# Optimization experiments

Hardware: AMD Instinct MI355X
Metric: run time of the kernel (lower is better)

Reference implementation:

```python
import jax, jax.numpy as jnp
import numpy as np

FEAT_DIM = 16
NUM_DEPTHS = 64


def _lookat(p):
    z = p / np.linalg.norm(p)
    up = np.array([0.0, 1.0, 0.0])
    x = np.cross(up, z); x = x / np.linalg.norm(x)
    y = np.cross(z, x)
    m = np.eye(4)
    m[:3, 0] = x; m[:3, 1] = y; m[:3, 2] = z; m[:3, 3] = p
    return m


def setup_inputs() -> dict:
    key = jax.random.key(0)
    ks = jax.random.split(key, 6)
    S, Vin, Vt, C, D, H, W = 2, 3, 4, FEAT_DIM, NUM_DEPTHS, 96, 96
    enc = jax.random.normal(ks[0], (S, Vin, C, D, H, W), jnp.float32) * 0.5
    rng = np.random.default_rng(0)

    def poses(n):
        ps = rng.normal(size=(S, n, 3))
        ps = ps / np.linalg.norm(ps, axis=-1, keepdims=True) * 1.3
        return jnp.asarray(np.stack([[_lookat(ps[i, j]) for j in range(n)] for i in range(S)]), jnp.float32)

    input_poses = poses(Vin)
    target_poses = poses(Vt)
    W1 = jax.random.normal(ks[1], (16, 64), jnp.float32) * 0.25
    W2 = jax.random.normal(ks[2], (64, 64), jnp.float32) * 0.125
    W3 = jax.random.normal(ks[3], (64, 17), jnp.float32) * 0.125
    return dict(
        encoded_imgs=enc, input_poses=input_poses, target_poses=target_poses,
        focal=1.2, z_near=0.8, z_far=1.8, samples_per_ray=64,
        W1=W1, b1=jnp.zeros((64,), jnp.float32),
        W2=W2, b2=jnp.zeros((64,), jnp.float32),
        W3=W3, b3=jnp.zeros((17,), jnp.float32),
    )


def grid_sample_3d(vol, grid):
    # vol: (N,C,D,H,W); grid: (N,P,3) xyz in [-1,1]; trilinear, zero padding, align_corners=False
    N, C, D, H, W = vol.shape
    P = grid.shape[1]
    ix = ((grid[..., 0] + 1.0) * W - 1.0) * 0.5
    iy = ((grid[..., 1] + 1.0) * H - 1.0) * 0.5
    iz = ((grid[..., 2] + 1.0) * D - 1.0) * 0.5
    x0, y0, z0 = jnp.floor(ix), jnp.floor(iy), jnp.floor(iz)
    volf = vol.reshape(N, C, D * H * W)
    out = jnp.zeros((N, C, P), vol.dtype)
    for dz in (0, 1):
        for dy in (0, 1):
            for dx in (0, 1):
                xc, yc, zc = x0 + dx, y0 + dy, z0 + dz
                wgt = (1.0 - jnp.abs(ix - xc)) * (1.0 - jnp.abs(iy - yc)) * (1.0 - jnp.abs(iz - zc))
                valid = ((xc >= 0) & (xc < W) & (yc >= 0) & (yc < H) & (zc >= 0) & (zc < D))
                xi = jnp.clip(xc, 0, W - 1).astype(jnp.int32)
                yi = jnp.clip(yc, 0, H - 1).astype(jnp.int32)
                zi = jnp.clip(zc, 0, D - 1).astype(jnp.int32)
                idx = (zi * H + yi) * W + xi  # (N,P)
                vals = jnp.take_along_axis(volf, idx[:, None, :], axis=2)  # (N,C,P)
                out = out + (wgt * valid)[:, None, :] * vals
    return out


def _upsample2_align_corners(x):
    # bilinear x2 on last two axes, align_corners=True (torch UpsamplingBilinear2d)
    def interp(x, axis):
        n = x.shape[axis]
        m = 2 * n
        pos = jnp.arange(m) * ((n - 1) / (m - 1))
        lo = jnp.floor(pos).astype(jnp.int32)
        hi = jnp.minimum(lo + 1, n - 1)
        f = (pos - lo).astype(x.dtype)
        xl = jnp.take(x, lo, axis=axis)
        xh = jnp.take(x, hi, axis=axis)
        shp = [1] * x.ndim; shp[axis] = m
        f = f.reshape(shp)
        return xl * (1.0 - f) + xh * f
    return interp(interp(x, -2), -1)


def _forward(encoded_imgs, input_poses, target_poses, focal, z_near, z_far,
             samples_per_ray, W1, b1, W2, b2, W3, b3):
    S, Vin, C, D, H, W = encoded_imgs.shape
    Vt = target_poses.shape[1]
    h, w = H // 2, W // 2
    spr = samples_per_ray
    dt = encoded_imgs.dtype

    # --- gen_rays at half resolution ---
    poses = target_poses.reshape(S * Vt, 4, 4)
    ys = ((jnp.arange(h, dtype=dt) + 0.5) / h) * 2.0 - 1.0
    xs = ((jnp.arange(w, dtype=dt) + 0.5) / w) * 2.0 - 1.0
    yy, xx = jnp.meshgrid(ys, xs, indexing='ij')
    dirs_cam = jnp.stack([xx / focal, -yy / focal, -jnp.ones_like(xx)], -1)  # (h,w,3)
    dirs = jnp.einsum('bij,hwj->bhwi', poses[:, :3, :3], dirs_cam)            # (B,h,w,3)
    origins = poses[:, None, None, :3, 3]                                      # (B,1,1,3)

    t = z_near + (z_far - z_near) * (jnp.arange(spr, dtype=dt) / (spr - 1))
    times = jnp.broadcast_to(t, (S * Vt, h, w, spr))
    pts = origins[..., None, :] + times[..., None] * dirs[..., None, :]        # (B,h,w,spr,3)

    times = times.reshape(S, Vt, h, w, spr)
    pts = pts.reshape(S, Vt, h, w, spr, 3)
    pts_h = jnp.concatenate([pts, jnp.ones_like(pts[..., :1])], axis=-1)      # (S,Vt,h,w,spr,4)

    # --- invert input poses (rigid) ---
    R = input_poses[..., :3, :3]
    tr = input_poses[..., :3, 3]
    Rt = jnp.swapaxes(R, -1, -2)
    inv_t = -jnp.einsum('svij,svj->svi', Rt, tr)
    top = jnp.concatenate([Rt, inv_t[..., None]], axis=-1)                     # (S,Vin,3,4)
    bottom = jnp.broadcast_to(jnp.array([0.0, 0.0, 0.0, 1.0], dt), (S, Vin, 1, 4))
    extrinsics = jnp.concatenate([top, bottom], axis=-2)                       # (S,Vin,4,4)

    local = jnp.einsum('svij,sthwpj->svthwpi', extrinsics, pts_h)              # (S,Vin,Vt,h,w,spr,4)
    x = local[..., 0]
    y = local[..., 1]
    z = -local[..., 2]
    u = x / z * focal
    v = y / z * focal
    min_z, max_z = focal * z_near, focal * z_far
    wd = 2.0 * (z - min_z) / (max_z - min_z) - 1.0
    uvw = jnp.stack((u, -v, -wd), axis=-1)                                     # (S,Vin,Vt,h,w,spr,3)

    feats = grid_sample_3d(encoded_imgs.reshape(S * Vin, C, D, H, W),
                           uvw.reshape(S * Vin, -1, 3))                        # (S*Vin,C,P)
    feats = feats.reshape(S, Vin, C, Vt, h, w, spr)
    feats = jnp.mean(feats, axis=1)                                            # baseline_mean camera weighting
    feats = jnp.transpose(feats, (0, 2, 3, 4, 5, 1))                           # (S,Vt,h,w,spr,C)

    # --- MLP with residual feature skip ---
    x1 = jax.nn.relu(feats @ W1 + b1)
    x2 = jax.nn.relu(x1 @ W2 + b2)
    out = x2 @ W3 + b3                                                         # (...,17)
    density = jax.nn.relu(out[..., 0])
    rgb = feats + out[..., 1:]

    # --- volume rendering ---
    deltas = times[..., 1:] - times[..., :-1]
    last = jnp.full_like(deltas[..., :1], 1e10)
    deltas = jnp.concatenate([deltas, last], axis=-1)
    sigdel = density * deltas
    alpha = 1.0 - jnp.exp(-sigdel)
    transmittance = jnp.exp(-jnp.cumsum(sigdel, axis=-1))
    wts = alpha * transmittance
    renders = jnp.sum(wts[..., None] * rgb, axis=-2)                           # (S,Vt,h,w,16)

    renders = jnp.transpose(renders, (0, 1, 4, 2, 3))                          # (S,Vt,16,h,w)
    renders = _upsample2_align_corners(renders.reshape(S * Vt, C, h, w))
    return renders.reshape(S, Vt, C, H, W)


def reference(encoded_imgs, input_poses, target_poses, focal, z_near, z_far,
              samples_per_ray, W1, b1, W2, b2, W3, b3):
    return _forward(encoded_imgs, input_poses, target_poses, float(focal), float(z_near),
                    float(z_far), int(samples_per_ray), W1, b1, W2, b2, W3, b3)
```

## Files before the change

### kernel.cpp

```cpp
#include <hip/hip_runtime.h>
#include <hip/hip_bf16.h>
#include <math.h>

#define NS   2
#define NVIN 3
#define NVT  4
#define NC   16
#define ND   64
#define NH   96
#define NW   96
#define HWH  48
#define SPR  64
#define DHW  (ND*NH*NW)
#define NTILE (DHW / 64)
#define NSAMP (NS*NVT*HWH*HWH*SPR)

typedef __attribute__((ext_vector_type(8))) short bfrag;
typedef __attribute__((ext_vector_type(4))) float cfrag;

#define MFMA16 __builtin_amdgcn_mfma_f32_16x16x32_bf16

__device__ __forceinline__ short f2bf(float x) {
    union { __hip_bfloat16 b; short s; } cv;
    cv.b = __float2bfloat16(x);
    return cv.s;
}
__device__ __forceinline__ float bf2f(short s) {
    union { unsigned int u; float f; } cv;
    cv.u = ((unsigned int)(unsigned short)s) << 16;
    return cv.f;
}

__device__ __forceinline__ void mk_frag(const float* p, bfrag& ah, bfrag& al) {
    float4 v0 = *(const float4*)p;
    float4 v1 = *(const float4*)(p + 4);
    float e[8] = {v0.x, v0.y, v0.z, v0.w, v1.x, v1.y, v1.z, v1.w};
    #pragma unroll
    for (int j = 0; j < 8; j++) {
        short h = f2bf(e[j]);
        ah[j] = h;
        al[j] = f2bf(e[j] - bf2f(h));
    }
}

__global__ __launch_bounds__(256) void wprep_kernel(
    const float* __restrict__ W1, const float* __restrict__ W2,
    const float* __restrict__ W3, short* __restrict__ whi, short* __restrict__ wlo)
{
    int t = blockIdx.x * 256 + threadIdx.x;
    int f = t >> 6, L = t & 63;
    int q = L >> 4, li = L & 15;
    #pragma unroll
    for (int j = 0; j < 8; j++) {
        int kloc = q * 8 + j;
        float w = 0.f;
        if (f < 4) {
            int n = f * 16 + li, k = kloc;
            if (k < 16) w = W1[k * 64 + n];
        } else if (f < 12) {
            int kt = (f - 4) >> 2, nt = (f - 4) & 3;
            w = W2[(kt * 32 + kloc) * 64 + nt * 16 + li];
        } else {
            int kt = (f - 12) >> 1, nt = (f - 12) & 1;
            int n = nt * 16 + li;
            if (n < 17) w = W3[(kt * 32 + kloc) * 17 + n];
        }
        short h = f2bf(w);
        whi[(f * 64 + L) * 8 + j] = h;
        wlo[(f * 64 + L) * 8 + j] = f2bf(w - bf2f(h));
    }
}

__global__ __launch_bounds__(256) void transpose_kernel(
    const float* __restrict__ in, float* __restrict__ out)
{
    __shared__ float tile[NC][64 + 4];
    const int t   = threadIdx.x;
    const int blk = blockIdx.x;
    const int vox0 = (blk % NTILE) * 64;
    const int sv   = blk / NTILE;

    const int c  = t >> 4;
    const int vg = (t & 15) * 4;
    const float* src = in + ((size_t)sv * NC + c) * DHW + vox0 + vg;
    float4 v = *(const float4*)src;
    tile[c][vg + 0] = v.x; tile[c][vg + 1] = v.y;
    tile[c][vg + 2] = v.z; tile[c][vg + 3] = v.w;
    __syncthreads();

    const int ov = t >> 2;
    const int oc = (t & 3) * 4;
    float4 w = make_float4(tile[oc + 0][ov], tile[oc + 1][ov],
                           tile[oc + 2][ov], tile[oc + 3][ov]);
    float* dst = out + ((size_t)sv * DHW + vox0 + ov) * NC + oc;
    *(float4*)dst = w;
}

__global__ __launch_bounds__(256) void gather_kernel(
    const float* __restrict__ enc_t,
    const float* __restrict__ ipose,
    const float* __restrict__ tpose,
    const float* __restrict__ focal_p,
    const float* __restrict__ znear_p,
    const float* __restrict__ zfar_p,
    float* __restrict__ xbuf)
{
    const int tid = blockIdx.x * 256 + threadIdx.x;
    const int c4  = tid & 3;
    const int smp = tid >> 2;
    const int d   = smp & 63;
    const int ray = smp >> 6;
    const int px  = ray % HWH;
    const int py  = (ray / HWH) % HWH;
    const int b   = ray / (HWH * HWH);
    const int s   = b >> 2;

    const float focal = focal_p[0];
    const float znear = znear_p[0];
    const float zfar  = zfar_p[0];

    const float* P = tpose + b * 16;
    float ysc = ((py + 0.5f) / (float)HWH) * 2.f - 1.f;
    float xsc = ((px + 0.5f) / (float)HWH) * 2.f - 1.f;
    float dcx = xsc / focal, dcy = -ysc / focal, dcz = -1.f;
    float dirx = P[0]*dcx + P[1]*dcy + P[2]*dcz;
    float diry = P[4]*dcx + P[5]*dcy + P[6]*dcz;
    float dirz = P[8]*dcx + P[9]*dcy + P[10]*dcz;

    float tv  = znear + (zfar - znear) * ((float)d / (float)(SPR - 1));
    float ptx = P[3] + tv * dirx, pty = P[7] + tv * diry, ptz = P[11] + tv * dirz;

    const float minz = focal * znear, maxz = focal * zfar;
    float f0 = 0.f, f1 = 0.f, f2 = 0.f, f3 = 0.f;

    for (int v = 0; v < NVIN; v++) {
        const float* E = ipose + (s * NVIN + v) * 16;
        float qx = ptx - E[3], qy = pty - E[7], qz = ptz - E[11];
        float lx = E[0]*qx + E[4]*qy + E[8]*qz;
        float ly = E[1]*qx + E[5]*qy + E[9]*qz;
        float lz = E[2]*qx + E[6]*qy + E[10]*qz;
        float zz = -lz;
        float u  = lx / zz * focal;
        float vv = ly / zz * focal;
        float wd = 2.f * (zz - minz) / (maxz - minz) - 1.f;
        float ix = ((u   + 1.f) * NW - 1.f) * 0.5f;
        float iy = ((-vv + 1.f) * NH - 1.f) * 0.5f;
        float iz = ((-wd + 1.f) * ND - 1.f) * 0.5f;
        float x0 = floorf(ix), y0 = floorf(iy), z0 = floorf(iz);

        const float* VB = enc_t + (size_t)(s * NVIN + v) * DHW * NC;
        #pragma unroll
        for (int k = 0; k < 8; k++) {
            float xc = x0 + (k & 1), yc = y0 + ((k >> 1) & 1), zc = z0 + (k >> 2);
            float wt = (1.f - fabsf(ix - xc)) * (1.f - fabsf(iy - yc)) * (1.f - fabsf(iz - zc));
            bool valid = (xc >= 0.f) && (xc < (float)NW) &&
                         (yc >= 0.f) && (yc < (float)NH) &&
                         (zc >= 0.f) && (zc < (float)ND);
            float w = valid ? wt : 0.f;
            int xi = min(max((int)xc, 0), NW - 1);
            int yi = min(max((int)yc, 0), NH - 1);
            int zi = min(max((int)zc, 0), ND - 1);
            int idx = (zi * NH + yi) * NW + xi;
            float4 a = *(const float4*)(VB + (size_t)idx * NC + c4 * 4);
            f0 += w * a.x; f1 += w * a.y; f2 += w * a.z; f3 += w * a.w;
        }
    }
    const float inv3 = 1.f / 3.f;
    ((float4*)xbuf)[tid] = make_float4(f0 * inv3, f1 * inv3, f2 * inv3, f3 * inv3);
}

__global__ __launch_bounds__(256) void mlp_kernel(
    const float* __restrict__ xbuf,
    const float* __restrict__ znear_p,
    const float* __restrict__ zfar_p,
    const short* __restrict__ whi, const short* __restrict__ wlo,
    const float* __restrict__ B1, const float* __restrict__ B2,
    const float* __restrict__ B3,
    float* __restrict__ rhalf)
{
    const int lane = threadIdx.x & 63;
    const int ray  = blockIdx.x * 4 + (threadIdx.x >> 6);
    const int px   = ray % HWH;
    const int py   = (ray / HWH) % HWH;
    const int b    = ray / (HWH * HWH);

    const float znear = znear_p[0];
    const float zfar  = zfar_p[0];

    __shared__ float sbuf[4][64][36];
    float (*B)[36] = sbuf[threadIdx.x >> 6];
    const int li = lane & 15, q = lane >> 4;
    const float* X = xbuf + (size_t)ray * 64 * NC;

    float b1v[4], b2v[4], b3v[2];
    #pragma unroll
    for (int nt = 0; nt < 4; nt++) { b1v[nt] = B1[nt*16 + li]; b2v[nt] = B2[nt*16 + li]; }
    b3v[0] = B3[li];
    b3v[1] = (li == 0) ? B3[16] : 0.f;

    bfrag xah[4], xal[4];
    bfrag zb = {0,0,0,0,0,0,0,0};
    #pragma unroll
    for (int mt = 0; mt < 4; mt++) {
        if (q < 2) mk_frag(X + (mt*16 + li) * NC + q * 8, xah[mt], xal[mt]);
        else { xah[mt] = zb; xal[mt] = zb; }
    }

    cfrag zc = {0.f, 0.f, 0.f, 0.f};
    cfrag h2acc[4][4];
    #pragma unroll
    for (int mt = 0; mt < 4; mt++)
        #pragma unroll
        for (int nt = 0; nt < 4; nt++) h2acc[mt][nt] = zc;

    #pragma unroll
    for (int c1 = 0; c1 < 2; c1++) {
        cfrag h1[4][2];
        #pragma unroll
        for (int nt2 = 0; nt2 < 2; nt2++) {
            int f = 2*c1 + nt2;
            bfrag bh = *(const bfrag*)(whi + (f*64 + lane)*8);
            bfrag bl = *(const bfrag*)(wlo + (f*64 + lane)*8);
            #pragma unroll
            for (int mt = 0; mt < 4; mt++) {
                cfrag a = zc;
                a = MFMA16(xal[mt], bh, a, 0, 0, 0);
                a = MFMA16(xah[mt], bl, a, 0, 0, 0);
                a = MFMA16(xah[mt], bh, a, 0, 0, 0);
                h1[mt][nt2] = a;
            }
        }
        __syncthreads();
        #pragma unroll
        for (int mt = 0; mt < 4; mt++)
            #pragma unroll
            for (int nt2 = 0; nt2 < 2; nt2++)
                #pragma unroll
                for (int r = 0; r < 4; r++)
                    B[mt*16 + q*4 + r][nt2*16 + li] =
                        fmaxf(h1[mt][nt2][r] + b1v[2*c1 + nt2], 0.f);
        __syncthreads();
        bfrag hah[4], hal[4];
        #pragma unroll
        for (int mt = 0; mt < 4; mt++)
            mk_frag(&B[mt*16 + li][q*8], hah[mt], hal[mt]);
        #pragma unroll
        for (int nt = 0; nt < 4; nt++) {
            int f = 4 + c1*4 + nt;
            bfrag bh = *(const bfrag*)(whi + (f*64 + lane)*8);
            bfrag bl = *(const bfrag*)(wlo + (f*64 + lane)*8);
            #pragma unroll
            for (int mt = 0; mt < 4; mt++) {
                cfrag a = h2acc[mt][nt];
                a = MFMA16(hal[mt], bh, a, 0, 0, 0);
                a = MFMA16(hah[mt], bl, a, 0, 0, 0);
                a = MFMA16(hah[mt], bh, a, 0, 0, 0);
                h2acc[mt][nt] = a;
            }
        }
    }

    cfrag oacc[4][2];
    #pragma unroll
    for (int mt = 0; mt < 4; mt++)
        #pragma unroll
        for (int nt = 0; nt < 2; nt++) oacc[mt][nt] = zc;

    #pragma unroll
    for (int c2 = 0; c2 < 2; c2++) {
        __syncthreads();
        #pragma unroll
        for (int mt = 0; mt < 4; mt++)
            #pragma unroll
            for (int nt2 = 0; nt2 < 2; nt2++)
                #pragma unroll
                for (int r = 0; r < 4; r++)
                    B[mt*16 + q*4 + r][nt2*16 + li] =
                        fmaxf(h2acc[mt][2*c2 + nt2][r] + b2v[2*c2 + nt2], 0.f);
        __syncthreads();
        bfrag hah[4], hal[4];
        #pragma unroll
        for (int mt = 0; mt < 4; mt++)
            mk_frag(&B[mt*16 + li][q*8], hah[mt], hal[mt]);
        #pragma unroll
        for (int nt = 0; nt < 2; nt++) {
            int f = 12 + c2*2 + nt;
            bfrag bh = *(const bfrag*)(whi + (f*64 + lane)*8);
            bfrag bl = *(const bfrag*)(wlo + (f*64 + lane)*8);
            #pragma unroll
            for (int mt = 0; mt < 4; mt++) {
                cfrag a = oacc[mt][nt];
                a = MFMA16(hal[mt], bh, a, 0, 0, 0);
                a = MFMA16(hah[mt], bl, a, 0, 0, 0);
                a = MFMA16(hah[mt], bh, a, 0, 0, 0);
                oacc[mt][nt] = a;
            }
        }
    }

    __syncthreads();
    #pragma unroll
    for (int mt = 0; mt < 4; mt++)
        #pragma unroll
        for (int nt = 0; nt < 2; nt++) {
            int ch = nt*16 + li;
            if (ch < 17) {
                #pragma unroll
                for (int r = 0; r < 4; r++)
                    B[mt*16 + q*4 + r][ch] = oacc[mt][nt][r] + b3v[nt];
            }
        }
    __syncthreads();
    float4 o0 = *(float4*)&B[lane][0];
    float4 o1 = *(float4*)&B[lane][4];
    float4 o2 = *(float4*)&B[lane][8];
    float4 o3 = *(float4*)&B[lane][12];
    float o16 = B[lane][16];

    float density = fmaxf(o0.x, 0.f);
    float orgb[16] = {o0.y, o0.z, o0.w, o1.x, o1.y, o1.z, o1.w, o2.x,
                      o2.y, o2.z, o2.w, o3.x, o3.y, o3.z, o3.w, o16};

    float4 fx0 = *(const float4*)(X + lane * NC + 0);
    float4 fx1 = *(const float4*)(X + lane * NC + 4);
    float4 fx2 = *(const float4*)(X + lane * NC + 8);
    float4 fx3 = *(const float4*)(X + lane * NC + 12);
    float feats[16] = {fx0.x, fx0.y, fx0.z, fx0.w, fx1.x, fx1.y, fx1.z, fx1.w,
                       fx2.x, fx2.y, fx2.z, fx2.w, fx3.x, fx3.y, fx3.z, fx3.w};

    float tv = znear + (zfar - znear) * ((float)lane / (float)(SPR - 1));
    float tn = znear + (zfar - znear) * ((float)(lane + 1) / (float)(SPR - 1));
    float delta = (lane < SPR - 1) ? (tn - tv) : 1e10f;
    float sigdel = density * delta;
    float alpha = 1.f - expf(-sigdel);
    float csum = sigdel;
    #pragma unroll
    for (int off = 1; off < 64; off <<= 1) {
        float nb = __shfl_up(csum, off, 64);
        if (lane >= off) csum += nb;
    }
    float wray = alpha * expf(-csum);

    #pragma unroll
    for (int c = 0; c < NC; c++) {
        float val = wray * (feats[c] + orgb[c]);
        #pragma unroll
        for (int off = 32; off >= 1; off >>= 1)
            val += __shfl_down(val, off, 64);
        if (lane == 0)
            rhalf[((b * NC + c) * HWH + py) * HWH + px] = val;
    }
}

__device__ __forceinline__ void mlp_and_composite(
    const float feats[NC], int lane, int b, int py, int px,
    float tv, float znear, float zfar,
    const float* __restrict__ W1, const float* __restrict__ B1,
    const float* __restrict__ W2, const float* __restrict__ B2,
    const float* __restrict__ W3, const float* __restrict__ B3,
    float* __restrict__ rhalf)
{
    float outa[17];
    #pragma unroll
    for (int c = 0; c < 17; c++) outa[c] = B3[c];
    for (int kc = 0; kc < 4; kc++) {
        float h2c[16];
        #pragma unroll
        for (int k = 0; k < 16; k++) h2c[k] = B2[kc * 16 + k];
        #pragma unroll 4
        for (int j = 0; j < 64; j++) {
            float a = B1[j];
            #pragma unroll
            for (int i = 0; i < NC; i++) a += feats[i] * W1[i * 64 + j];
            a = fmaxf(a, 0.f);
            const float* w2p = W2 + j * 64 + kc * 16;
            #pragma unroll
            for (int k = 0; k < 16; k++) h2c[k] += a * w2p[k];
        }
        #pragma unroll
        for (int k = 0; k < 16; k++) {
            float hv = fmaxf(h2c[k], 0.f);
            const float* w3p = W3 + (kc * 16 + k) * 17;
            #pragma unroll
            for (int c = 0; c < 17; c++) outa[c] += hv * w3p[c];
        }
    }
    float density = fmaxf(outa[0], 0.f);
    float tn = znear + (zfar - znear) * ((float)(lane + 1) / (float)(SPR - 1));
    float delta = (lane < SPR - 1) ? (tn - tv) : 1e10f;
    float sigdel = density * delta;
    float alpha = 1.f - expf(-sigdel);
    float csum = sigdel;
    #pragma unroll
    for (int off = 1; off < 64; off <<= 1) {
        float nb = __shfl_up(csum, off, 64);
        if (lane >= off) csum += nb;
    }
    float wray = alpha * expf(-csum);
    #pragma unroll
    for (int c = 0; c < NC; c++) {
        float val = wray * (feats[c] + outa[1 + c]);
        #pragma unroll
        for (int off = 32; off >= 1; off >>= 1)
            val += __shfl_down(val, off, 64);
        if (lane == 0)
            rhalf[((b * NC + c) * HWH + py) * HWH + px] = val;
    }
}

__global__ __launch_bounds__(256) void render_kernel(
    const float* __restrict__ enc,
    const float* __restrict__ ipose,
    const float* __restrict__ tpose,
    const float* __restrict__ focal_p,
    const float* __restrict__ znear_p,
    const float* __restrict__ zfar_p,
    const float* __restrict__ W1, const float* __restrict__ B1,
    const float* __restrict__ W2, const float* __restrict__ B2,
    const float* __restrict__ W3, const float* __restrict__ B3,
    float* __restrict__ rhalf)
{
    const int lane = threadIdx.x & 63;
    const int ray  = blockIdx.x * 4 + (threadIdx.x >> 6);
    const int px   = ray % HWH;
    const int py   = (ray / HWH) % HWH;
    const int b    = ray / (HWH * HWH);
    const int s    = b >> 2;
    const float focal = focal_p[0];
    const float znear = znear_p[0];
    const float zfar  = zfar_p[0];
    const float* P = tpose + b * 16;
    float ysc = ((py + 0.5f) / (float)HWH) * 2.f - 1.f;
    float xsc = ((px + 0.5f) / (float)HWH) * 2.f - 1.f;
    float dcx = xsc / focal, dcy = -ysc / focal, dcz = -1.f;
    float dirx = P[0]*dcx + P[1]*dcy + P[2]*dcz;
    float diry = P[4]*dcx + P[5]*dcy + P[6]*dcz;
    float dirz = P[8]*dcx + P[9]*dcy + P[10]*dcz;
    float tv  = znear + (zfar - znear) * ((float)lane / (float)(SPR - 1));
    float ptx = P[3] + tv * dirx, pty = P[7] + tv * diry, ptz = P[11] + tv * dirz;
    float feats[NC];
    #pragma unroll
    for (int c = 0; c < NC; c++) feats[c] = 0.f;
    const float minz = focal * znear, maxz = focal * zfar;
    for (int v = 0; v < NVIN; v++) {
        const float* E = ipose + (s * NVIN + v) * 16;
        float qx = ptx - E[3], qy = pty - E[7], qz = ptz - E[11];
        float lx = E[0]*qx + E[4]*qy + E[8]*qz;
        float ly = E[1]*qx + E[5]*qy + E[9]*qz;
        float lz = E[2]*qx + E[6]*qy + E[10]*qz;
        float zz = -lz;
        float u  = lx / zz * focal;
        float vv = ly / zz * focal;
        float wd = 2.f * (zz - minz) / (maxz - minz) - 1.f;
        float ix = ((u   + 1.f) * NW - 1.f) * 0.5f;
        float iy = ((-vv + 1.f) * NH - 1.f) * 0.5f;
        float iz = ((-wd + 1.f) * ND - 1.f) * 0.5f;
        float x0 = floorf(ix), y0 = floorf(iy), z0 = floorf(iz);
        float wgt[8]; int idx[8];
        #pragma unroll
        for (int k = 0; k < 8; k++) {
            float xc = x0 + (k & 1), yc = y0 + ((k >> 1) & 1), zc = z0 + (k >> 2);
            float wt = (1.f - fabsf(ix - xc)) * (1.f - fabsf(iy - yc)) * (1.f - fabsf(iz - zc));
            bool valid = (xc >= 0.f) && (xc < (float)NW) &&
                         (yc >= 0.f) && (yc < (float)NH) &&
                         (zc >= 0.f) && (zc < (float)ND);
            wgt[k] = valid ? wt : 0.f;
            int xi = min(max((int)xc, 0), NW - 1);
            int yi = min(max((int)yc, 0), NH - 1);
            int zi = min(max((int)zc, 0), ND - 1);
            idx[k] = (zi * NH + yi) * NW + xi;
        }
        const float* VB = enc + (size_t)(s * NVIN + v) * NC * DHW;
        #pragma unroll
        for (int c = 0; c < NC; c++) {
            const float* vc = VB + c * DHW;
            float acc = 0.f;
            #pragma unroll
            for (int k = 0; k < 8; k++) acc += wgt[k] * vc[idx[k]];
            feats[c] += acc;
        }
    }
    #pragma unroll
    for (int c = 0; c < NC; c++) feats[c] *= (1.f / 3.f);
    mlp_and_composite(feats, lane, b, py, px, tv, znear, zfar,
                      W1, B1, W2, B2, W3, B3, rhalf);
}

__global__ __launch_bounds__(256) void upsample_kernel(
    const float* __restrict__ in, float* __restrict__ out)
{
    int tid = blockIdx.x * 256 + threadIdx.x;
    int ox = tid % NW;
    int oy = (tid / NW) % NH;
    int c  = (tid / (NW * NH)) % NC;
    int b  = tid / (NW * NH * NC);
    const float sc = (float)((HWH - 1) / (double)(NH - 1));
    float pyf = oy * sc;
    float pxf = ox * sc;
    int y0 = (int)floorf(pyf); int y1 = min(y0 + 1, HWH - 1); float fy = pyf - y0;
    int x0 = (int)floorf(pxf); int x1 = min(x0 + 1, HWH - 1); float fx = pxf - x0;
    const float* src = in + (b * NC + c) * HWH * HWH;
    float v00 = src[y0 * HWH + x0], v01 = src[y0 * HWH + x1];
    float v10 = src[y1 * HWH + x0], v11 = src[y1 * HWH + x1];
    float gl = v00 * (1.f - fy) + v10 * fy;
    float gr = v01 * (1.f - fy) + v11 * fy;
    out[tid] = gl * (1.f - fx) + gr * fx;
}

extern "C" void kernel_launch(void* const* d_in, const int* in_sizes, int n_in,
                              void* d_out, int out_size, void* d_ws, size_t ws_size,
                              hipStream_t stream) {
    const float* enc   = (const float*)d_in[0];
    const float* ipose = (const float*)d_in[1];
    const float* tpose = (const float*)d_in[2];
    const float* focal = (const float*)d_in[3];
    const float* znear = (const float*)d_in[4];
    const float* zfar  = (const float*)d_in[5];
    const float* W1 = (const float*)d_in[7];
    const float* B1 = (const float*)d_in[8];
    const float* W2 = (const float*)d_in[9];
    const float* B2 = (const float*)d_in[10];
    const float* W3 = (const float*)d_in[11];
    const float* B3 = (const float*)d_in[12];

    float* out = (float*)d_out;
    const int nrays = NS * NVT * HWH * HWH;
    const int nout  = NS * NVT * NC * NH * NW;
    const size_t enc_t_bytes = (size_t)NS * NVIN * NC * DHW * 4;
    const size_t rhalf_bytes = (size_t)nrays * NC * 4;
    const size_t wfrag_bytes = 16 * 64 * 8 * sizeof(short);
    const size_t xbuf_bytes  = (size_t)NSAMP * NC * 4;

    if (ws_size >= enc_t_bytes + rhalf_bytes + 2 * wfrag_bytes + xbuf_bytes) {
        char* base = (char*)d_ws;
        float* enc_t = (float*)base;                      base += enc_t_bytes;
        float* rhalf = (float*)base;                      base += rhalf_bytes;
        short* whi   = (short*)base;                      base += wfrag_bytes;
        short* wlo   = (short*)base;                      base += wfrag_bytes;
        float* xbuf  = (float*)base;

        wprep_kernel<<<4, 256, 0, stream>>>(W1, W2, W3, whi, wlo);
        transpose_kernel<<<NS * NVIN * NTILE, 256, 0, stream>>>(enc, enc_t);
        gather_kernel<<<NSAMP * 4 / 256, 256, 0, stream>>>(
            enc_t, ipose, tpose, focal, znear, zfar, xbuf);
        mlp_kernel<<<nrays / 4, 256, 0, stream>>>(
            xbuf, znear, zfar, whi, wlo, B1, B2, B3, rhalf);
        upsample_kernel<<<nout / 256, 256, 0, stream>>>(rhalf, out);
    } else {
        float* rhalf = (float*)d_ws;
        render_kernel<<<nrays / 4, 256, 0, stream>>>(
            enc, ipose, tpose, focal, znear, zfar,
            W1, B1, W2, B2, W3, B3, rhalf);
        upsample_kernel<<<nout / 256, 256, 0, stream>>>(rhalf, out);
    }
}
```

Measured before the change: 616.3 us.

## Fuse gather and MLP into one kernel with per-wave LDS staging

Result: slower. 652.4 us (+5.9%).

```diff
diff --git a/kernel.cpp b/kernel.cpp
--- a/kernel.cpp
+++ b/kernel.cpp
@@ -19,6 +19,8 @@
 typedef __attribute__((ext_vector_type(4))) float cfrag;
 
 #define MFMA16 __builtin_amdgcn_mfma_f32_16x16x32_bf16
+
+#define WAVE_LDS_SYNC() asm volatile("s_waitcnt lgkmcnt(0)" ::: "memory")
 
 __device__ __forceinline__ short f2bf(float x) {
     union { __hip_bfloat16 b; short s; } cv;
@@ -96,81 +98,13 @@
     *(float4*)dst = w;
 }
 
-__global__ __launch_bounds__(256) void gather_kernel(
+#define XSTRIDE 20
+
+__global__ __launch_bounds__(256) void fused_kernel(
     const float* __restrict__ enc_t,
     const float* __restrict__ ipose,
     const float* __restrict__ tpose,
     const float* __restrict__ focal_p,
-    const float* __restrict__ znear_p,
-    const float* __restrict__ zfar_p,
-    float* __restrict__ xbuf)
-{
-    const int tid = blockIdx.x * 256 + threadIdx.x;
-    const int c4  = tid & 3;
-    const int smp = tid >> 2;
-    const int d   = smp & 63;
-    const int ray = smp >> 6;
-    const int px  = ray % HWH;
-    const int py  = (ray / HWH) % HWH;
-    const int b   = ray / (HWH * HWH);
-    const int s   = b >> 2;
-
-    const float focal = focal_p[0];
-    const float znear = znear_p[0];
-    const float zfar  = zfar_p[0];
-
-    const float* P = tpose + b * 16;
-    float ysc = ((py + 0.5f) / (float)HWH) * 2.f - 1.f;
-    float xsc = ((px + 0.5f) / (float)HWH) * 2.f - 1.f;
-    float dcx = xsc / focal, dcy = -ysc / focal, dcz = -1.f;
-    float dirx = P[0]*dcx + P[1]*dcy + P[2]*dcz;
-    float diry = P[4]*dcx + P[5]*dcy + P[6]*dcz;
-    float dirz = P[8]*dcx + P[9]*dcy + P[10]*dcz;
-
-    float tv  = znear + (zfar - znear) * ((float)d / (float)(SPR - 1));
-    float ptx = P[3] + tv * dirx, pty = P[7] + tv * diry, ptz = P[11] + tv * dirz;
-
-    const float minz = focal * znear, maxz = focal * zfar;
-    float f0 = 0.f, f1 = 0.f, f2 = 0.f, f3 = 0.f;
-
-    for (int v = 0; v < NVIN; v++) {
-        const float* E = ipose + (s * NVIN + v) * 16;
-        float qx = ptx - E[3], qy = pty - E[7], qz = ptz - E[11];
-        float lx = E[0]*qx + E[4]*qy + E[8]*qz;
-        float ly = E[1]*qx + E[5]*qy + E[9]*qz;
-        float lz = E[2]*qx + E[6]*qy + E[10]*qz;
-        float zz = -lz;
-        float u  = lx / zz * focal;
-        float vv = ly / zz * focal;
-        float wd = 2.f * (zz - minz) / (maxz - minz) - 1.f;
-        float ix = ((u   + 1.f) * NW - 1.f) * 0.5f;
-        float iy = ((-vv + 1.f) * NH - 1.f) * 0.5f;
-        float iz = ((-wd + 1.f) * ND - 1.f) * 0.5f;
-        float x0 = floorf(ix), y0 = floorf(iy), z0 = floorf(iz);
-
-        const float* VB = enc_t + (size_t)(s * NVIN + v) * DHW * NC;
-        #pragma unroll
-        for (int k = 0; k < 8; k++) {
-            float xc = x0 + (k & 1), yc = y0 + ((k >> 1) & 1), zc = z0 + (k >> 2);
-            float wt = (1.f - fabsf(ix - xc)) * (1.f - fabsf(iy - yc)) * (1.f - fabsf(iz - zc));
-            bool valid = (xc >= 0.f) && (xc < (float)NW) &&
-                         (yc >= 0.f) && (yc < (float)NH) &&
-                         (zc >= 0.f) && (zc < (float)ND);
-            float w = valid ? wt : 0.f;
-            int xi = min(max((int)xc, 0), NW - 1);
-            int yi = min(max((int)yc, 0), NH - 1);
-            int zi = min(max((int)zc, 0), ND - 1);
-            int idx = (zi * NH + yi) * NW + xi;
-            float4 a = *(const float4*)(VB + (size_t)idx * NC + c4 * 4);
-            f0 += w * a.x; f1 += w * a.y; f2 += w * a.z; f3 += w * a.w;
-        }
-    }
-    const float inv3 = 1.f / 3.f;
-    ((float4*)xbuf)[tid] = make_float4(f0 * inv3, f1 * inv3, f2 * inv3, f3 * inv3);
-}
-
-__global__ __launch_bounds__(256) void mlp_kernel(
-    const float* __restrict__ xbuf,
     const float* __restrict__ znear_p,
     const float* __restrict__ zfar_p,
     const short* __restrict__ whi, const short* __restrict__ wlo,
@@ -179,18 +113,90 @@
     float* __restrict__ rhalf)
 {
     const int lane = threadIdx.x & 63;
-    const int ray  = blockIdx.x * 4 + (threadIdx.x >> 6);
+    const int wv   = threadIdx.x >> 6;
+    const int ray  = blockIdx.x * 4 + wv;
     const int px   = ray % HWH;
     const int py   = (ray / HWH) % HWH;
     const int b    = ray / (HWH * HWH);
-
+    const int s    = b >> 2;
+
+    const float focal = focal_p[0];
     const float znear = znear_p[0];
     const float zfar  = zfar_p[0];
 
-    __shared__ float sbuf[4][64][36];
-    float (*B)[36] = sbuf[threadIdx.x >> 6];
+    __shared__ float sbuf[4][64 * 36];
+    float* Wb = sbuf[wv];
+    float* Xs = sbuf[wv];
+
+    const float* P = tpose + b * 16;
+    float ysc = ((py + 0.5f) / (float)HWH) * 2.f - 1.f;
+    float xsc = ((px + 0.5f) / (float)HWH) * 2.f - 1.f;
+    float dcx = xsc / focal, dcy = -ysc / focal, dcz = -1.f;
+    float dirx = P[0]*dcx + P[1]*dcy + P[2]*dcz;
+    float diry = P[4]*dcx + P[5]*dcy + P[6]*dcz;
+    float dirz = P[8]*dcx + P[9]*dcy + P[10]*dcz;
+
+    float lox[NVIN], loy[NVIN], loz[NVIN];
+    float ldx[NVIN], ldy[NVIN], ldz[NVIN];
+    #pragma unroll
+    for (int v = 0; v < NVIN; v++) {
+        const float* E = ipose + (s * NVIN + v) * 16;
+        float qx = P[3] - E[3], qy = P[7] - E[7], qz = P[11] - E[11];
+        lox[v] = E[0]*qx + E[4]*qy + E[8]*qz;
+        loy[v] = E[1]*qx + E[5]*qy + E[9]*qz;
+        loz[v] = E[2]*qx + E[6]*qy + E[10]*qz;
+        ldx[v] = E[0]*dirx + E[4]*diry + E[8]*dirz;
+        ldy[v] = E[1]*dirx + E[5]*diry + E[9]*dirz;
+        ldz[v] = E[2]*dirx + E[6]*diry + E[10]*dirz;
+    }
+
+    const float minz = focal * znear, maxz = focal * zfar;
+    const int  c4    = lane & 3;
+    const int  dbase = lane >> 2;
+    const float inv3 = 1.f / 3.f;
+
+    #pragma unroll 1
+    for (int i = 0; i < 4; i++) {
+        int d = dbase + i * 16;
+        float tv = znear + (zfar - znear) * ((float)d / (float)(SPR - 1));
+        float f0 = 0.f, f1 = 0.f, f2 = 0.f, f3 = 0.f;
+        #pragma unroll
+        for (int v = 0; v < NVIN; v++) {
+            float lx = lox[v] + tv * ldx[v];
+            float ly = loy[v] + tv * ldy[v];
+            float lz = loz[v] + tv * ldz[v];
+            float zz = -lz;
+            float u  = lx / zz * focal;
+            float vvv = ly / zz * focal;
+            float wd = 2.f * (zz - minz) / (maxz - minz) - 1.f;
+            float ix = ((u    + 1.f) * NW - 1.f) * 0.5f;
+            float iy = ((-vvv + 1.f) * NH - 1.f) * 0.5f;
+            float iz = ((-wd  + 1.f) * ND - 1.f) * 0.5f;
+            float x0 = floorf(ix), y0 = floorf(iy), z0 = floorf(iz);
+
+            const float* VB = enc_t + (size_t)(s * NVIN + v) * DHW * NC;
+            #pragma unroll
+            for (int k = 0; k < 8; k++) {
+                float xc = x0 + (k & 1), yc = y0 + ((k >> 1) & 1), zc = z0 + (k >> 2);
+                float wt = (1.f - fabsf(ix - xc)) * (1.f - fabsf(iy - yc)) * (1.f - fabsf(iz - zc));
+                bool valid = (xc >= 0.f) && (xc < (float)NW) &&
+                             (yc >= 0.f) && (yc < (float)NH) &&
+                             (zc >= 0.f) && (zc < (float)ND);
+                float w = valid ? wt : 0.f;
+                int xi = min(max((int)xc, 0), NW - 1);
+                int yi = min(max((int)yc, 0), NH - 1);
+                int zi = min(max((int)zc, 0), ND - 1);
+                int idx = (zi * NH + yi) * NW + xi;
+                float4 a = *(const float4*)(VB + (size_t)idx * NC + c4 * 4);
+                f0 += w * a.x; f1 += w * a.y; f2 += w * a.z; f3 += w * a.w;
+            }
+        }
+        *(float4*)&Xs[d * XSTRIDE + c4 * 4] =
+            make_float4(f0 * inv3, f1 * inv3, f2 * inv3, f3 * inv3);
+    }
+    WAVE_LDS_SYNC();
+
     const int li = lane & 15, q = lane >> 4;
-    const float* X = xbuf + (size_t)ray * 64 * NC;
 
     float b1v[4], b2v[4], b3v[2];
     #pragma unroll
@@ -198,13 +204,19 @@
     b3v[0] = B3[li];
     b3v[1] = (li == 0) ? B3[16] : 0.f;
 
+    float4 fx0 = *(const float4*)&Xs[lane * XSTRIDE + 0];
+    float4 fx1 = *(const float4*)&Xs[lane * XSTRIDE + 4];
+    float4 fx2 = *(const float4*)&Xs[lane * XSTRIDE + 8];
+    float4 fx3 = *(const float4*)&Xs[lane * XSTRIDE + 12];
+
     bfrag xah[4], xal[4];
     bfrag zb = {0,0,0,0,0,0,0,0};
     #pragma unroll
     for (int mt = 0; mt < 4; mt++) {
-        if (q < 2) mk_frag(X + (mt*16 + li) * NC + q * 8, xah[mt], xal[mt]);
+        if (q < 2) mk_frag(&Xs[(mt*16 + li) * XSTRIDE + q * 8], xah[mt], xal[mt]);
         else { xah[mt] = zb; xal[mt] = zb; }
     }
+    WAVE_LDS_SYNC();
 
     cfrag zc = {0.f, 0.f, 0.f, 0.f};
     cfrag h2acc[4][4];
@@ -230,20 +242,20 @@
                 h1[mt][nt2] = a;
             }
         }
-        __syncthreads();
+        WAVE_LDS_SYNC();
         #pragma unroll
         for (int mt = 0; mt < 4; mt++)
             #pragma unroll
             for (int nt2 = 0; nt2 < 2; nt2++)
                 #pragma unroll
                 for (int r = 0; r < 4; r++)
-                    B[mt*16 + q*4 + r][nt2*16 + li] =
+                    Wb[(mt*16 + q*4 + r)*36 + nt2*16 + li] =
                         fmaxf(h1[mt][nt2][r] + b1v[2*c1 + nt2], 0.f);
-        __syncthreads();
+        WAVE_LDS_SYNC();
         bfrag hah[4], hal[4];
         #pragma unroll
         for (int mt = 0; mt < 4; mt++)
-            mk_frag(&B[mt*16 + li][q*8], hah[mt], hal[mt]);
+            mk_frag(&Wb[(mt*16 + li)*36 + q*8], hah[mt], hal[mt]);
         #pragma unroll
         for (int nt = 0; nt < 4; nt++) {
             int f = 4 + c1*4 + nt;
@@ -268,20 +280,20 @@
 
     #pragma unroll
     for (int c2 = 0; c2 < 2; c2++) {
-        __syncthreads();
+        WAVE_LDS_SYNC();
         #pragma unroll
         for (int mt = 0; mt < 4; mt++)
             #pragma unroll
             for (int nt2 = 0; nt2 < 2; nt2++)
                 #pragma unroll
                 for (int r = 0; r < 4; r++)
-                    B[mt*16 + q*4 + r][nt2*16 + li] =
+                    Wb[(mt*16 + q*4 + r)*36 + nt2*16 + li] =
                         fmaxf(h2acc[mt][2*c2 + nt2][r] + b2v[2*c2 + nt2], 0.f);
-        __syncthreads();
+        WAVE_LDS_SYNC();
         bfrag hah[4], hal[4];
         #pragma unroll
         for (int mt = 0; mt < 4; mt++)
-            mk_frag(&B[mt*16 + li][q*8], hah[mt], hal[mt]);
+            mk_frag(&Wb[(mt*16 + li)*36 + q*8], hah[mt], hal[mt]);
         #pragma unroll
         for (int nt = 0; nt < 2; nt++) {
             int f = 12 + c2*2 + nt;
@@ -298,7 +310,7 @@
         }
     }
 
-    __syncthreads();
+    WAVE_LDS_SYNC();
     #pragma unroll
     for (int mt = 0; mt < 4; mt++)
         #pragma unroll
@@ -307,24 +319,19 @@
             if (ch < 17) {
                 #pragma unroll
                 for (int r = 0; r < 4; r++)
-                    B[mt*16 + q*4 + r][ch] = oacc[mt][nt][r] + b3v[nt];
+                    Wb[(mt*16 + q*4 + r)*36 + ch] = oacc[mt][nt][r] + b3v[nt];
             }
         }
-    __syncthreads();
-    float4 o0 = *(float4*)&B[lane][0];
-    float4 o1 = *(float4*)&B[lane][4];
-    float4 o2 = *(float4*)&B[lane][8];
-    float4 o3 = *(float4*)&B[lane][12];
-    float o16 = B[lane][16];
+    WAVE_LDS_SYNC();
+    float4 o0 = *(float4*)&Wb[lane*36 + 0];
+    float4 o1 = *(float4*)&Wb[lane*36 + 4];
+    float4 o2 = *(float4*)&Wb[lane*36 + 8];
+    float4 o3 = *(float4*)&Wb[lane*36 + 12];
+    float o16 = Wb[lane*36 + 16];
 
     float density = fmaxf(o0.x, 0.f);
     float orgb[16] = {o0.y, o0.z, o0.w, o1.x, o1.y, o1.z, o1.w, o2.x,
                       o2.y, o2.z, o2.w, o3.x, o3.y, o3.z, o3.w, o16};
-
-    float4 fx0 = *(const float4*)(X + lane * NC + 0);
-    float4 fx1 = *(const float4*)(X + lane * NC + 4);
-    float4 fx2 = *(const float4*)(X + lane * NC + 8);
-    float4 fx3 = *(const float4*)(X + lane * NC + 12);
     float feats[16] = {fx0.x, fx0.y, fx0.z, fx0.w, fx1.x, fx1.y, fx1.z, fx1.w,
                        fx2.x, fx2.y, fx2.z, fx2.w, fx3.x, fx3.y, fx3.z, fx3.w};
 
@@ -529,22 +536,18 @@
     const size_t enc_t_bytes = (size_t)NS * NVIN * NC * DHW * 4;
     const size_t rhalf_bytes = (size_t)nrays * NC * 4;
     const size_t wfrag_bytes = 16 * 64 * 8 * sizeof(short);
-    const size_t xbuf_bytes  = (size_t)NSAMP * NC * 4;
-
-    if (ws_size >= enc_t_bytes + rhalf_bytes + 2 * wfrag_bytes + xbuf_bytes) {
+
+    if (ws_size >= enc_t_bytes + rhalf_bytes + 2 * wfrag_bytes) {
         char* base = (char*)d_ws;
         float* enc_t = (float*)base;                      base += enc_t_bytes;
         float* rhalf = (float*)base;                      base += rhalf_bytes;
         short* whi   = (short*)base;                      base += wfrag_bytes;
-        short* wlo   = (short*)base;                      base += wfrag_bytes;
-        float* xbuf  = (float*)base;
+        short* wlo   = (short*)base;
 
         wprep_kernel<<<4, 256, 0, stream>>>(W1, W2, W3, whi, wlo);
         transpose_kernel<<<NS * NVIN * NTILE, 256, 0, stream>>>(enc, enc_t);
-        gather_kernel<<<NSAMP * 4 / 256, 256, 0, stream>>>(
-            enc_t, ipose, tpose, focal, znear, zfar, xbuf);
-        mlp_kernel<<<nrays / 4, 256, 0, stream>>>(
-            xbuf, znear, zfar, whi, wlo, B1, B2, B3, rhalf);
+        fused_kernel<<<nrays / 4, 256, 0, stream>>>(
+            enc_t, ipose, tpose, focal, znear, zfar, whi, wlo, B1, B2, B3, rhalf);
         upsample_kernel<<<nout / 256, 256, 0, stream>>>(rhalf, out);
     } else {
         float* rhalf = (float*)d_ws;
```
